# Optimization experiments

Measured on AMD Instinct MI355X. Metric: run time of the kernel, lower is better.

Reference implementation:

```python
import jax, jax.numpy as jnp
import numpy as np

DEPTH = 4
DIM = 1024
HEADS = 16
DIM_HEAD = 64
INNER = HEADS * DIM_HEAD  # 1024
MLP = 4096
CTX = 768
SCALE = DIM_HEAD ** -0.5
EPS = 1e-5


def setup_inputs() -> dict:
    key = jax.random.key(0)
    ks = jax.random.split(key, 12)
    def rn(k, shape, s=0.02):
        return jax.random.normal(k, shape, jnp.float32) * s
    return {
        "x": jax.random.normal(ks[0], (2, 2048, DIM), jnp.float32),
        "context": jax.random.normal(ks[1], (2, 1024, CTX), jnp.float32),
        "ln1_g": jnp.ones((DEPTH, DIM), jnp.float32),
        "ln1_b": jnp.zeros((DEPTH, DIM), jnp.float32),
        "w_qkv": rn(ks[2], (DEPTH, DIM, 3 * INNER)),
        "w_sa_o": rn(ks[3], (DEPTH, INNER, DIM)),
        "b_sa_o": jnp.zeros((DEPTH, DIM), jnp.float32),
        "ln2_g": jnp.ones((DEPTH, DIM), jnp.float32),
        "ln2_b": jnp.zeros((DEPTH, DIM), jnp.float32),
        "w_q": rn(ks[4], (DEPTH, DIM, INNER)),
        "w_kv": rn(ks[5], (DEPTH, CTX, 2 * INNER)),
        "w_ca_o": rn(ks[6], (DEPTH, INNER, DIM)),
        "b_ca_o": jnp.zeros((DEPTH, DIM), jnp.float32),
        "ln3_g": jnp.ones((DEPTH, DIM), jnp.float32),
        "ln3_b": jnp.zeros((DEPTH, DIM), jnp.float32),
        "w_ff1": rn(ks[7], (DEPTH, DIM, MLP)),
        "b_ff1": jnp.zeros((DEPTH, MLP), jnp.float32),
        "w_ff2": rn(ks[8], (DEPTH, MLP, DIM)),
        "b_ff2": jnp.zeros((DEPTH, DIM), jnp.float32),
    }


def _ln(x, g, b):
    mu = jnp.mean(x, axis=-1, keepdims=True)
    var = jnp.mean(jnp.square(x - mu), axis=-1, keepdims=True)
    return (x - mu) * jax.lax.rsqrt(var + EPS) * g + b


def _heads(t):
    # [b, n, h*d] -> [b, h, n, d]
    b, n, _ = t.shape
    return t.reshape(b, n, HEADS, DIM_HEAD).transpose(0, 2, 1, 3)


def _mha(q, k, v):
    # q,k,v: [b, h, n, d]; naive matmul-softmax-matmul, same math as the torch code
    attn = jax.nn.softmax(jnp.einsum('bhqd,bhkd->bhqk', q, k) * SCALE, axis=-1)
    out = jnp.einsum('bhqk,bhkd->bhqd', attn, v)
    b, h, n, d = out.shape
    return out.transpose(0, 2, 1, 3).reshape(b, n, h * d)


def reference(x, context, ln1_g, ln1_b, w_qkv, w_sa_o, b_sa_o,
              ln2_g, ln2_b, w_q, w_kv, w_ca_o, b_ca_o,
              ln3_g, ln3_b, w_ff1, b_ff1, w_ff2, b_ff2):
    for i in range(DEPTH):
        # self-attention
        h = _ln(x, ln1_g[i], ln1_b[i])
        qkv = h @ w_qkv[i]
        q, k, v = jnp.split(qkv, 3, axis=-1)
        sa = _mha(_heads(q), _heads(k), _heads(v)) @ w_sa_o[i] + b_sa_o[i]
        x = sa + x
        # cross-attention
        h = _ln(x, ln2_g[i], ln2_b[i])
        q = h @ w_q[i]
        kv = context @ w_kv[i]
        k, v = jnp.split(kv, 2, axis=-1)
        ca = _mha(_heads(q), _heads(k), _heads(v)) @ w_ca_o[i] + b_ca_o[i]
        x = ca + x
        # feed-forward (exact GELU, matching torch nn.GELU default)
        h = _ln(x, ln3_g[i], ln3_b[i])
        ff = jax.nn.gelu(h @ w_ff1[i] + b_ff1[i], approximate=False) @ w_ff2[i] + b_ff2[i]
        x = ff + x
    return x
```

## Files before the change

kernel.cpp:

```cpp
#include <hip/hip_runtime.h>
#include <hip/hip_bf16.h>
#include <math.h>

typedef __bf16 bf16_t;
typedef __bf16 bf16x8 __attribute__((ext_vector_type(8)));
typedef __bf16 bf16x4 __attribute__((ext_vector_type(4)));
typedef float f32x4 __attribute__((ext_vector_type(4)));
typedef float f32x16 __attribute__((ext_vector_type(16)));
typedef unsigned short u16;
typedef unsigned int u32;
typedef u16 u16x8 __attribute__((ext_vector_type(8)));
typedef u32 u32x4 __attribute__((ext_vector_type(4)));

#define NDEPTH 4
#define DIM 1024
#define NHEADS 16
#define MLP_DIM 4096
#define CTXD 768
#define NTOK 4096
#define NCTX 2048
#define ATT_SC2 0.18033688011112042f

__device__ inline void gload_lds16(const void* g, void* l) {
  __builtin_amdgcn_global_load_lds(
      (const __attribute__((address_space(1))) void*)g,
      (__attribute__((address_space(3))) void*)l, 16, 0, 0);
}

__device__ inline u32 packbf2(float a, float b) {
  union { bf16_t h[2]; u32 w; } u;
  u.h[0] = (bf16_t)a; u.h[1] = (bf16_t)b;
  return u.w;
}

template<int EPI>
__device__ inline void epi_store(void* outp, const float* bias, const float* res,
                                 int row, int col, int N, float v) {
  size_t idx = (size_t)row * N + col;
  if (EPI == 3) {
    ((float*)outp)[idx] = v + bias[col] + res[idx];
  } else if (EPI == 2) {
    float vb = v + bias[col];
    ((bf16_t*)outp)[idx] = (bf16_t)(0.5f * vb * (1.f + erff(vb * 0.70710678118f)));
  } else {
    ((bf16_t*)outp)[idx] = (bf16_t)v;
  }
}

template<int EPI>
__global__ __launch_bounds__(512) void gemm_bf16(
    const bf16_t* __restrict__ A, const bf16_t* __restrict__ Bt,
    const float* __restrict__ bias, const float* __restrict__ res,
    void* __restrict__ outp, int M, int N, int K)
{
  __shared__ alignas(16) bf16_t As[3][128 * 32];
  __shared__ alignas(16) bf16_t Bs[3][128 * 32];
  const int tid = threadIdx.x, lane = tid & 63, wave = tid >> 6;
  const int bx = blockIdx.x, by = blockIdx.y;
  const int wr = wave >> 2, wc = wave & 3;
  const int l15 = lane & 15, l4 = lane >> 4;

  const bf16_t* Ag = A + (size_t)by * 128 * K;
  const bf16_t* Bg = Bt + (size_t)bx * 128 * K;

  f32x4 acc[4][2] = {};

  const int srow = tid >> 2, soff = (tid & 3) * 8;
  auto stage = [&](int buf, int k0) {
    gload_lds16(Ag + (size_t)srow * K + k0 + soff, &As[buf][(size_t)tid * 8]);
    gload_lds16(Bg + (size_t)srow * K + k0 + soff, &Bs[buf][(size_t)tid * 8]);
  };

  const int nk = K >> 5;
  stage(0, 0);
  stage(1, 32);
  asm volatile("s_waitcnt vmcnt(2)" ::: "memory");
  __builtin_amdgcn_s_barrier();
  __builtin_amdgcn_sched_barrier(0);

  for (int t = 0; t < nk; ++t) {
    const int cur = t % 3;
    if (t + 2 < nk) stage((t + 2) % 3, (t + 2) << 5);

    bf16x8 af[4], bfr[2];
#pragma unroll
    for (int mi = 0; mi < 4; ++mi)
      af[mi] = *(const bf16x8*)&As[cur][(wr * 64 + mi * 16 + l15) * 32 + l4 * 8];
#pragma unroll
    for (int ni = 0; ni < 2; ++ni)
      bfr[ni] = *(const bf16x8*)&Bs[cur][(wc * 32 + ni * 16 + l15) * 32 + l4 * 8];
#pragma unroll
    for (int mi = 0; mi < 4; ++mi)
#pragma unroll
      for (int ni = 0; ni < 2; ++ni)
        acc[mi][ni] = __builtin_amdgcn_mfma_f32_16x16x32_bf16(af[mi], bfr[ni], acc[mi][ni], 0, 0, 0);

    if (t + 2 < nk) {
      asm volatile("s_waitcnt vmcnt(2)" ::: "memory");
    } else if (t + 1 < nk) {
      asm volatile("s_waitcnt vmcnt(0)" ::: "memory");
    } else {
      break;
    }
    __builtin_amdgcn_s_barrier();
    __builtin_amdgcn_sched_barrier(0);
  }

  const int r0 = by * 128 + wr * 64, c0 = bx * 128 + wc * 32;
#pragma unroll
  for (int ni = 0; ni < 2; ++ni)
#pragma unroll
    for (int mi = 0; mi < 4; ++mi)
#pragma unroll
      for (int r = 0; r < 4; ++r)
        epi_store<EPI>(outp, bias, res, r0 + mi * 16 + l4 * 4 + r,
                       c0 + ni * 16 + l15, N, acc[mi][ni][r]);
}

template<int EPI>
__global__ __launch_bounds__(256) void gemm64_bf16(
    const bf16_t* __restrict__ A, const bf16_t* __restrict__ Bt,
    const float* __restrict__ bias, const float* __restrict__ res,
    void* __restrict__ outp, int M, int N, int K)
{
  __shared__ alignas(16) bf16_t As[3][64 * 32];
  __shared__ alignas(16) bf16_t Bs[3][64 * 32];
  const int tid = threadIdx.x, lane = tid & 63, wave = tid >> 6;
  const int bx = blockIdx.x, by = blockIdx.y;
  const int wr = wave >> 1, wc = wave & 1;
  const int l15 = lane & 15, l4 = lane >> 4;

  const bf16_t* Ag = A + (size_t)by * 64 * K;
  const bf16_t* Bg = Bt + (size_t)bx * 64 * K;

  f32x4 acc[2][2] = {};

  const int srow = tid >> 2, soff = (tid & 3) * 8;
  auto stage = [&](int buf, int k0) {
    gload_lds16(Ag + (size_t)srow * K + k0 + soff, &As[buf][(size_t)tid * 8]);
    gload_lds16(Bg + (size_t)srow * K + k0 + soff, &Bs[buf][(size_t)tid * 8]);
  };

  const int nk = K >> 5;
  stage(0, 0);
  stage(1, 32);
  asm volatile("s_waitcnt vmcnt(2)" ::: "memory");
  __builtin_amdgcn_s_barrier();
  __builtin_amdgcn_sched_barrier(0);

  for (int t = 0; t < nk; ++t) {
    const int cur = t % 3;
    if (t + 2 < nk) stage((t + 2) % 3, (t + 2) << 5);

    bf16x8 af[2], bfr[2];
#pragma unroll
    for (int mi = 0; mi < 2; ++mi)
      af[mi] = *(const bf16x8*)&As[cur][(wr * 32 + mi * 16 + l15) * 32 + l4 * 8];
#pragma unroll
    for (int ni = 0; ni < 2; ++ni)
      bfr[ni] = *(const bf16x8*)&Bs[cur][(wc * 32 + ni * 16 + l15) * 32 + l4 * 8];
#pragma unroll
    for (int mi = 0; mi < 2; ++mi)
#pragma unroll
      for (int ni = 0; ni < 2; ++ni)
        acc[mi][ni] = __builtin_amdgcn_mfma_f32_16x16x32_bf16(af[mi], bfr[ni], acc[mi][ni], 0, 0, 0);

    if (t + 2 < nk) {
      asm volatile("s_waitcnt vmcnt(2)" ::: "memory");
    } else if (t + 1 < nk) {
      asm volatile("s_waitcnt vmcnt(0)" ::: "memory");
    } else {
      break;
    }
    __builtin_amdgcn_s_barrier();
    __builtin_amdgcn_sched_barrier(0);
  }

  const int r0 = by * 64 + wr * 32, c0 = bx * 64 + wc * 32;
#pragma unroll
  for (int ni = 0; ni < 2; ++ni)
#pragma unroll
    for (int mi = 0; mi < 2; ++mi)
#pragma unroll
      for (int r = 0; r < 4; ++r)
        epi_store<EPI>(outp, bias, res, r0 + mi * 16 + l4 * 4 + r,
                       c0 + ni * 16 + l15, N, acc[mi][ni][r]);
}

__global__ __launch_bounds__(256) void attn_fwd(
    const bf16_t* __restrict__ Q, int qs,
    const bf16_t* __restrict__ K, const bf16_t* __restrict__ V, int kvs,
    bf16_t* __restrict__ O, int os, int nq, int nk)
{
  __shared__ bf16_t Ks[2][64][72];
  __shared__ bf16_t Vt[2][64][72];

  const int tid = threadIdx.x, lane = tid & 63, wv = tid >> 6;
  const int l31 = lane & 31, hi = lane >> 5;
  const int h = blockIdx.y, bz = blockIdx.z;
  const size_t qrow0 = (size_t)bz * nq + (size_t)blockIdx.x * 128 + wv * 32;
  const bf16_t* Qb = Q + qrow0 * qs + h * 64;
  const bf16_t* Kb = K + (size_t)bz * nk * kvs + h * 64;
  const bf16_t* Vb = V + (size_t)bz * nk * kvs + h * 64;
  bf16_t* Ob = O + qrow0 * os + h * 64;

  bf16x8 qa[4];
#pragma unroll
  for (int c = 0; c < 4; ++c)
    qa[c] = *(const bf16x8*)(Qb + (size_t)l31 * qs + c * 16 + hi * 8);

  const int krow = tid >> 2, kcol = (tid & 3) * 16;
  const int vd = tid & 63, vkb = tid >> 6;

  u16x8 kreg[2], vreg[2];
  auto load_tile = [&](int kt) {
#pragma unroll
    for (int i = 0; i < 2; ++i)
      kreg[i] = *(const u16x8*)(Kb + (size_t)(kt * 64 + krow) * kvs + kcol + i * 8);
#pragma unroll
    for (int i = 0; i < 2; ++i) {
      u16x8 t;
#pragma unroll
      for (int j = 0; j < 8; ++j)
        t[j] = *(const u16*)(Vb + (size_t)(kt * 64 + vkb * 16 + i * 8 + j) * kvs + vd);
      vreg[i] = t;
    }
  };
  auto store_tile = [&](int buf) {
#pragma unroll
    for (int i = 0; i < 2; ++i)
      *(u16x8*)&Ks[buf][krow][kcol + i * 8] = kreg[i];
#pragma unroll
    for (int i = 0; i < 2; ++i)
      *(u16x8*)&Vt[buf][vd][vkb * 16 + i * 8] = vreg[i];
  };

  float m_run2 = -1e30f, l_run = 0.f;
  f32x16 acc[2] = {};

  const int ntiles = nk >> 6;
  load_tile(0);
  store_tile(0);
  __syncthreads();

  for (int kt = 0; kt < ntiles; ++kt) {
    const int cur = kt & 1;
    const bool pre = (kt + 1 < ntiles);
    if (pre) load_tile(kt + 1);

    f32x16 s[2] = {};
    __builtin_amdgcn_s_setprio(1);
#pragma unroll
    for (int kb = 0; kb < 2; ++kb)
#pragma unroll
      for (int c = 0; c < 4; ++c) {
        bf16x8 kf = *(const bf16x8*)&Ks[cur][kb * 32 + l31][c * 16 + hi * 8];
        s[kb] = __builtin_amdgcn_mfma_f32_32x32x16_bf16(kf, qa[c], s[kb], 0, 0, 0);
      }
    __builtin_amdgcn_s_setprio(0);

    float smax = s[0][0];
#pragma unroll
    for (int kb = 0; kb < 2; ++kb)
#pragma unroll
      for (int r = 0; r < 16; ++r) smax = fmaxf(smax, s[kb][r]);
    smax *= ATT_SC2;
    smax = fmaxf(smax, __shfl_xor(smax, 32));

    if (!__all(smax <= m_run2 + 11.0f)) {
      const float mn = fmaxf(m_run2, smax);
      const float esc = exp2f(m_run2 - mn);
      m_run2 = mn;
      l_run *= esc;
#pragma unroll
      for (int r = 0; r < 16; ++r) {
        int q = (r & 3) + 8 * (r >> 2) + 4 * hi;
        float eq = __shfl(esc, q);
        acc[0][r] *= eq;
        acc[1][r] *= eq;
      }
    }

    float psum = 0.f;
    u32x4 paw[2][2];
#pragma unroll
    for (int kb = 0; kb < 2; ++kb) {
      float pv[16];
#pragma unroll
      for (int r = 0; r < 16; ++r) {
        pv[r] = exp2f(s[kb][r] * ATT_SC2 - m_run2);
        psum += pv[r];
      }
#pragma unroll
      for (int h2 = 0; h2 < 2; ++h2) {
        u32 a0 = packbf2(pv[h2 * 8 + 0], pv[h2 * 8 + 1]);
        u32 a1 = packbf2(pv[h2 * 8 + 2], pv[h2 * 8 + 3]);
        u32 a2 = packbf2(pv[h2 * 8 + 4], pv[h2 * 8 + 5]);
        u32 a3 = packbf2(pv[h2 * 8 + 6], pv[h2 * 8 + 7]);
        asm volatile("v_permlane32_swap_b32 %0, %1" : "+v"(a0), "+v"(a2));
        asm volatile("v_permlane32_swap_b32 %0, %1" : "+v"(a1), "+v"(a3));
        paw[kb][h2][0] = a0; paw[kb][h2][1] = a1;
        paw[kb][h2][2] = a2; paw[kb][h2][3] = a3;
      }
    }
    psum += __shfl_xor(psum, 32);
    l_run += psum;

    __builtin_amdgcn_s_setprio(1);
#pragma unroll
    for (int kb = 0; kb < 2; ++kb)
#pragma unroll
      for (int h2 = 0; h2 < 2; ++h2) {
        union { u32x4 w; bf16x8 v; } pu;
        pu.w = paw[kb][h2];
#pragma unroll
        for (int dblk = 0; dblk < 2; ++dblk) {
          bf16x8 vb = *(const bf16x8*)&Vt[cur][dblk * 32 + l31][kb * 32 + h2 * 16 + hi * 8];
          acc[dblk] = __builtin_amdgcn_mfma_f32_32x32x16_bf16(pu.v, vb, acc[dblk], 0, 0, 0);
        }
      }
    __builtin_amdgcn_s_setprio(0);

    if (pre) store_tile(cur ^ 1);
    __syncthreads();
  }

#pragma unroll
  for (int r = 0; r < 16; ++r) {
    int q = (r & 3) + 8 * (r >> 2) + 4 * hi;
    float lq = __shfl(l_run, q);
    float inv = 1.f / lq;
#pragma unroll
    for (int dblk = 0; dblk < 2; ++dblk)
      Ob[(size_t)q * os + dblk * 32 + l31] = (bf16_t)(acc[dblk][r] * inv);
  }
}

__global__ __launch_bounds__(256) void layernorm_f32_bf16(
    const float* __restrict__ x, const float* __restrict__ g, const float* __restrict__ b,
    bf16_t* __restrict__ out)
{
  const int row = blockIdx.x, tid = threadIdx.x;
  const float4 v = ((const float4*)(x + (size_t)row * 1024))[tid];
  float s = v.x + v.y + v.z + v.w;
  float s2 = v.x * v.x + v.y * v.y + v.z * v.z + v.w * v.w;
#pragma unroll
  for (int off = 32; off > 0; off >>= 1) {
    s += __shfl_down(s, off);
    s2 += __shfl_down(s2, off);
  }
  __shared__ float ps[4], ps2[4];
  const int lane = tid & 63, wave = tid >> 6;
  if (lane == 0) { ps[wave] = s; ps2[wave] = s2; }
  __syncthreads();
  s = ps[0] + ps[1] + ps[2] + ps[3];
  s2 = ps2[0] + ps2[1] + ps2[2] + ps2[3];
  const float mu = s * (1.f / 1024.f);
  const float var = s2 * (1.f / 1024.f) - mu * mu;
  const float rstd = rsqrtf(var + 1e-5f);
  const float4 gv = ((const float4*)g)[tid];
  const float4 bv = ((const float4*)b)[tid];
  bf16x4 o;
  o[0] = (bf16_t)((v.x - mu) * rstd * gv.x + bv.x);
  o[1] = (bf16_t)((v.y - mu) * rstd * gv.y + bv.y);
  o[2] = (bf16_t)((v.z - mu) * rstd * gv.z + bv.z);
  o[3] = (bf16_t)((v.w - mu) * rstd * gv.w + bv.w);
  *(bf16x4*)(out + (size_t)row * 1024 + tid * 4) = o;
}

__global__ void transpose_to_bf16(const float* __restrict__ src, bf16_t* __restrict__ dst, int K, int N)
{
  __shared__ float tile[32][33];
  const size_t loff = (size_t)blockIdx.z * K * N;
  src += loff; dst += loff;
  const int k0 = blockIdx.y * 32, n0 = blockIdx.x * 32;
  const int tx = threadIdx.x, ty = threadIdx.y;
#pragma unroll
  for (int i = ty; i < 32; i += 8)
    tile[i][tx] = src[(size_t)(k0 + i) * N + n0 + tx];
  __syncthreads();
#pragma unroll
  for (int i = ty; i < 32; i += 8)
    dst[(size_t)(n0 + i) * K + k0 + tx] = (bf16_t)tile[tx][i];
}

__global__ void f32_to_bf16(const float* __restrict__ src, bf16_t* __restrict__ dst, int n4)
{
  int i = blockIdx.x * blockDim.x + threadIdx.x;
  if (i < n4) {
    float4 v = ((const float4*)src)[i];
    bf16x4 o;
    o[0] = (bf16_t)v.x; o[1] = (bf16_t)v.y; o[2] = (bf16_t)v.z; o[3] = (bf16_t)v.w;
    ((bf16x4*)dst)[i] = o;
  }
}

__global__ void copy_f32(const float* __restrict__ src, float* __restrict__ dst, int n4)
{
  int i = blockIdx.x * blockDim.x + threadIdx.x;
  if (i < n4) ((float4*)dst)[i] = ((const float4*)src)[i];
}

extern "C" void kernel_launch(void* const* d_in, const int* in_sizes, int n_in,
                              void* d_out, int out_size, void* d_ws, size_t ws_size,
                              hipStream_t stream)
{
  const float* x      = (const float*)d_in[0];
  const float* ctx    = (const float*)d_in[1];
  const float* ln1_g  = (const float*)d_in[2];
  const float* ln1_b  = (const float*)d_in[3];
  const float* w_qkv  = (const float*)d_in[4];
  const float* w_sa_o = (const float*)d_in[5];
  const float* b_sa_o = (const float*)d_in[6];
  const float* ln2_g  = (const float*)d_in[7];
  const float* ln2_b  = (const float*)d_in[8];
  const float* w_q    = (const float*)d_in[9];
  const float* w_kv   = (const float*)d_in[10];
  const float* w_ca_o = (const float*)d_in[11];
  const float* b_ca_o = (const float*)d_in[12];
  const float* ln3_g  = (const float*)d_in[13];
  const float* ln3_b  = (const float*)d_in[14];
  const float* w_ff1  = (const float*)d_in[15];
  const float* b_ff1  = (const float*)d_in[16];
  const float* w_ff2  = (const float*)d_in[17];
  const float* b_ff2  = (const float*)d_in[18];

  char* p = (char*)d_ws;
  auto alloc = [&](size_t bytes) { char* r = p; p += (bytes + 255) & ~(size_t)255; return r; };
  bf16_t* wqkv_t = (bf16_t*)alloc((size_t)NDEPTH * 3072 * 1024 * 2);
  bf16_t* wsao_t = (bf16_t*)alloc((size_t)NDEPTH * 1024 * 1024 * 2);
  bf16_t* wq_t   = (bf16_t*)alloc((size_t)NDEPTH * 1024 * 1024 * 2);
  bf16_t* wkv_t  = (bf16_t*)alloc((size_t)NDEPTH * 2048 * 768 * 2);
  bf16_t* wcao_t = (bf16_t*)alloc((size_t)NDEPTH * 1024 * 1024 * 2);
  bf16_t* wff1_t = (bf16_t*)alloc((size_t)NDEPTH * 4096 * 1024 * 2);
  bf16_t* wff2_t = (bf16_t*)alloc((size_t)NDEPTH * 1024 * 4096 * 2);
  bf16_t* ctxb   = (bf16_t*)alloc((size_t)NCTX * CTXD * 2);
  float*  xbuf   = (float*)alloc((size_t)NTOK * DIM * 4);
  bf16_t* lnbuf  = (bf16_t*)alloc((size_t)NTOK * DIM * 2);
  bf16_t* bigbuf = (bf16_t*)alloc((size_t)NTOK * 4096 * 2);
  bf16_t* qbuf   = (bf16_t*)alloc((size_t)NTOK * DIM * 2);
  bf16_t* kvbuf  = (bf16_t*)alloc((size_t)NCTX * 2048 * 2);
  if ((size_t)(p - (char*)d_ws) > ws_size) return;

  dim3 tb(32, 8);
  transpose_to_bf16<<<dim3(3072 / 32, 1024 / 32, NDEPTH), tb, 0, stream>>>(w_qkv, wqkv_t, 1024, 3072);
  transpose_to_bf16<<<dim3(1024 / 32, 1024 / 32, NDEPTH), tb, 0, stream>>>(w_sa_o, wsao_t, 1024, 1024);
  transpose_to_bf16<<<dim3(1024 / 32, 1024 / 32, NDEPTH), tb, 0, stream>>>(w_q, wq_t, 1024, 1024);
  transpose_to_bf16<<<dim3(2048 / 32, 768 / 32, NDEPTH), tb, 0, stream>>>(w_kv, wkv_t, 768, 2048);
  transpose_to_bf16<<<dim3(1024 / 32, 1024 / 32, NDEPTH), tb, 0, stream>>>(w_ca_o, wcao_t, 1024, 1024);
  transpose_to_bf16<<<dim3(4096 / 32, 1024 / 32, NDEPTH), tb, 0, stream>>>(w_ff1, wff1_t, 1024, 4096);
  transpose_to_bf16<<<dim3(1024 / 32, 4096 / 32, NDEPTH), tb, 0, stream>>>(w_ff2, wff2_t, 4096, 1024);
  f32_to_bf16<<<(NCTX * CTXD / 4 + 255) / 256, 256, 0, stream>>>(ctx, ctxb, NCTX * CTXD / 4);
  copy_f32<<<(NTOK * DIM / 4 + 255) / 256, 256, 0, stream>>>(x, xbuf, NTOK * DIM / 4);

  for (int i = 0; i < NDEPTH; ++i) {
    layernorm_f32_bf16<<<NTOK, 256, 0, stream>>>(xbuf, ln1_g + i * DIM, ln1_b + i * DIM, lnbuf);
    gemm_bf16<0><<<dim3(3072 / 128, NTOK / 128), 512, 0, stream>>>(
        lnbuf, wqkv_t + (size_t)i * 3072 * 1024, nullptr, nullptr, bigbuf, NTOK, 3072, 1024);
    attn_fwd<<<dim3(2048 / 128, NHEADS, 2), 256, 0, stream>>>(
        bigbuf, 3072, bigbuf + 1024, bigbuf + 2048, 3072, lnbuf, 1024, 2048, 2048);
    gemm64_bf16<3><<<dim3(1024 / 64, NTOK / 64), 256, 0, stream>>>(
        lnbuf, wsao_t + (size_t)i * 1024 * 1024, b_sa_o + i * DIM, xbuf, xbuf, NTOK, 1024, 1024);
    layernorm_f32_bf16<<<NTOK, 256, 0, stream>>>(xbuf, ln2_g + i * DIM, ln2_b + i * DIM, lnbuf);
    gemm64_bf16<0><<<dim3(1024 / 64, NTOK / 64), 256, 0, stream>>>(
        lnbuf, wq_t + (size_t)i * 1024 * 1024, nullptr, nullptr, qbuf, NTOK, 1024, 1024);
    gemm64_bf16<0><<<dim3(2048 / 64, NCTX / 64), 256, 0, stream>>>(
        ctxb, wkv_t + (size_t)i * 2048 * 768, nullptr, nullptr, kvbuf, NCTX, 2048, 768);
    attn_fwd<<<dim3(2048 / 128, NHEADS, 2), 256, 0, stream>>>(
        qbuf, 1024, kvbuf, kvbuf + 1024, 2048, lnbuf, 1024, 2048, 1024);
    gemm64_bf16<3><<<dim3(1024 / 64, NTOK / 64), 256, 0, stream>>>(
        lnbuf, wcao_t + (size_t)i * 1024 * 1024, b_ca_o + i * DIM, xbuf, xbuf, NTOK, 1024, 1024);
    layernorm_f32_bf16<<<NTOK, 256, 0, stream>>>(xbuf, ln3_g + i * DIM, ln3_b + i * DIM, lnbuf);
    gemm_bf16<2><<<dim3(4096 / 128, NTOK / 128), 512, 0, stream>>>(
        lnbuf, wff1_t + (size_t)i * 4096 * 1024, b_ff1 + i * MLP_DIM, nullptr, bigbuf, NTOK, 4096, 1024);
    gemm64_bf16<3><<<dim3(1024 / 64, NTOK / 64), 256, 0, stream>>>(
        bigbuf, wff2_t + (size_t)i * 1024 * 4096, b_ff2 + i * DIM, xbuf, xbuf, NTOK, 1024, 4096);
  }
  copy_f32<<<(NTOK * DIM / 4 + 255) / 256, 256, 0, stream>>>(xbuf, (float*)d_out, NTOK * DIM / 4);
}
```

Baseline: 1.830 ms.

## Split attention KV tiles across wave pairs and merge partial softmax states

```diff
diff --git a/kernel.cpp b/kernel.cpp
--- a/kernel.cpp
+++ b/kernel.cpp
@@ -197,8 +197,9 @@
 
   const int tid = threadIdx.x, lane = tid & 63, wv = tid >> 6;
   const int l31 = lane & 31, hi = lane >> 5;
+  const int pair = wv >> 1, sK = wv & 1;
   const int h = blockIdx.y, bz = blockIdx.z;
-  const size_t qrow0 = (size_t)bz * nq + (size_t)blockIdx.x * 128 + wv * 32;
+  const size_t qrow0 = (size_t)bz * nq + (size_t)blockIdx.x * 64 + pair * 32;
   const bf16_t* Qb = Q + qrow0 * qs + h * 64;
   const bf16_t* Kb = K + (size_t)bz * nk * kvs + h * 64;
   const bf16_t* Vb = V + (size_t)bz * nk * kvs + h * 64;
@@ -248,22 +249,18 @@
     const bool pre = (kt + 1 < ntiles);
     if (pre) load_tile(kt + 1);
 
-    f32x16 s[2] = {};
+    f32x16 s = {};
     __builtin_amdgcn_s_setprio(1);
 #pragma unroll
-    for (int kb = 0; kb < 2; ++kb)
-#pragma unroll
-      for (int c = 0; c < 4; ++c) {
-        bf16x8 kf = *(const bf16x8*)&Ks[cur][kb * 32 + l31][c * 16 + hi * 8];
-        s[kb] = __builtin_amdgcn_mfma_f32_32x32x16_bf16(kf, qa[c], s[kb], 0, 0, 0);
-      }
+    for (int c = 0; c < 4; ++c) {
+      bf16x8 kf = *(const bf16x8*)&Ks[cur][sK * 32 + l31][c * 16 + hi * 8];
+      s = __builtin_amdgcn_mfma_f32_32x32x16_bf16(kf, qa[c], s, 0, 0, 0);
+    }
     __builtin_amdgcn_s_setprio(0);
 
-    float smax = s[0][0];
-#pragma unroll
-    for (int kb = 0; kb < 2; ++kb)
-#pragma unroll
-      for (int r = 0; r < 16; ++r) smax = fmaxf(smax, s[kb][r]);
+    float smax = s[0];
+#pragma unroll
+    for (int r = 1; r < 16; ++r) smax = fmaxf(smax, s[r]);
     smax *= ATT_SC2;
     smax = fmaxf(smax, __shfl_xor(smax, 32));
 
@@ -282,57 +279,75 @@
     }
 
     float psum = 0.f;
-    u32x4 paw[2][2];
-#pragma unroll
-    for (int kb = 0; kb < 2; ++kb) {
-      float pv[16];
-#pragma unroll
-      for (int r = 0; r < 16; ++r) {
-        pv[r] = exp2f(s[kb][r] * ATT_SC2 - m_run2);
-        psum += pv[r];
-      }
-#pragma unroll
-      for (int h2 = 0; h2 < 2; ++h2) {
-        u32 a0 = packbf2(pv[h2 * 8 + 0], pv[h2 * 8 + 1]);
-        u32 a1 = packbf2(pv[h2 * 8 + 2], pv[h2 * 8 + 3]);
-        u32 a2 = packbf2(pv[h2 * 8 + 4], pv[h2 * 8 + 5]);
-        u32 a3 = packbf2(pv[h2 * 8 + 6], pv[h2 * 8 + 7]);
-        asm volatile("v_permlane32_swap_b32 %0, %1" : "+v"(a0), "+v"(a2));
-        asm volatile("v_permlane32_swap_b32 %0, %1" : "+v"(a1), "+v"(a3));
-        paw[kb][h2][0] = a0; paw[kb][h2][1] = a1;
-        paw[kb][h2][2] = a2; paw[kb][h2][3] = a3;
-      }
+    float pv[16];
+#pragma unroll
+    for (int r = 0; r < 16; ++r) {
+      pv[r] = exp2f(s[r] * ATT_SC2 - m_run2);
+      psum += pv[r];
     }
     psum += __shfl_xor(psum, 32);
     l_run += psum;
 
+    u32x4 paw[2];
+#pragma unroll
+    for (int h2 = 0; h2 < 2; ++h2) {
+      u32 a0 = packbf2(pv[h2 * 8 + 0], pv[h2 * 8 + 1]);
+      u32 a1 = packbf2(pv[h2 * 8 + 2], pv[h2 * 8 + 3]);
+      u32 a2 = packbf2(pv[h2 * 8 + 4], pv[h2 * 8 + 5]);
+      u32 a3 = packbf2(pv[h2 * 8 + 6], pv[h2 * 8 + 7]);
+      asm volatile("v_permlane32_swap_b32 %0, %1" : "+v"(a0), "+v"(a2));
+      asm volatile("v_permlane32_swap_b32 %0, %1" : "+v"(a1), "+v"(a3));
+      paw[h2][0] = a0; paw[h2][1] = a1; paw[h2][2] = a2; paw[h2][3] = a3;
+    }
+
     __builtin_amdgcn_s_setprio(1);
 #pragma unroll
-    for (int kb = 0; kb < 2; ++kb)
-#pragma unroll
-      for (int h2 = 0; h2 < 2; ++h2) {
-        union { u32x4 w; bf16x8 v; } pu;
-        pu.w = paw[kb][h2];
-#pragma unroll
-        for (int dblk = 0; dblk < 2; ++dblk) {
-          bf16x8 vb = *(const bf16x8*)&Vt[cur][dblk * 32 + l31][kb * 32 + h2 * 16 + hi * 8];
-          acc[dblk] = __builtin_amdgcn_mfma_f32_32x32x16_bf16(pu.v, vb, acc[dblk], 0, 0, 0);
-        }
+    for (int h2 = 0; h2 < 2; ++h2) {
+      union { u32x4 w; bf16x8 v; } pu;
+      pu.w = paw[h2];
+#pragma unroll
+      for (int dblk = 0; dblk < 2; ++dblk) {
+        bf16x8 vb = *(const bf16x8*)&Vt[cur][dblk * 32 + l31][sK * 32 + h2 * 16 + hi * 8];
+        acc[dblk] = __builtin_amdgcn_mfma_f32_32x32x16_bf16(pu.v, vb, acc[dblk], 0, 0, 0);
       }
+    }
     __builtin_amdgcn_s_setprio(0);
 
     if (pre) store_tile(cur ^ 1);
     __syncthreads();
   }
 
-#pragma unroll
-  for (int r = 0; r < 16; ++r) {
-    int q = (r & 3) + 8 * (r >> 2) + 4 * hi;
-    float lq = __shfl(l_run, q);
-    float inv = 1.f / lq;
+  float* mb = (float*)&Ks[0][0][0];
+  float* ml = (float*)&Vt[0][0][0];
+  if (sK == 1) {
 #pragma unroll
     for (int dblk = 0; dblk < 2; ++dblk)
-      Ob[(size_t)q * os + dblk * 32 + l31] = (bf16_t)(acc[dblk][r] * inv);
+#pragma unroll
+      for (int r = 0; r < 16; ++r)
+        mb[((pair * 2 + dblk) * 16 + r) * 64 + lane] = acc[dblk][r];
+    if (lane < 32) {
+      ml[(pair * 2 + 0) * 32 + lane] = m_run2;
+      ml[(pair * 2 + 1) * 32 + lane] = l_run;
+    }
+  }
+  __syncthreads();
+  if (sK == 0) {
+    float m1 = ml[(pair * 2 + 0) * 32 + l31];
+    float l1 = ml[(pair * 2 + 1) * 32 + l31];
+    float mm = fmaxf(m_run2, m1);
+    float f0 = exp2f(m_run2 - mm), f1 = exp2f(m1 - mm);
+    float inv = 1.f / (l_run * f0 + l1 * f1);
+#pragma unroll
+    for (int r = 0; r < 16; ++r) {
+      int q = (r & 3) + 8 * (r >> 2) + 4 * hi;
+      float f0r = __shfl(f0, q), f1r = __shfl(f1, q), invr = __shfl(inv, q);
+#pragma unroll
+      for (int dblk = 0; dblk < 2; ++dblk) {
+        float o = (acc[dblk][r] * f0r +
+                   mb[((pair * 2 + dblk) * 16 + r) * 64 + lane] * f1r) * invr;
+        Ob[(size_t)q * os + dblk * 32 + l31] = (bf16_t)o;
+      }
+    }
   }
 }
 
@@ -457,7 +472,7 @@
     layernorm_f32_bf16<<<NTOK, 256, 0, stream>>>(xbuf, ln1_g + i * DIM, ln1_b + i * DIM, lnbuf);
     gemm_bf16<0><<<dim3(3072 / 128, NTOK / 128), 512, 0, stream>>>(
         lnbuf, wqkv_t + (size_t)i * 3072 * 1024, nullptr, nullptr, bigbuf, NTOK, 3072, 1024);
-    attn_fwd<<<dim3(2048 / 128, NHEADS, 2), 256, 0, stream>>>(
+    attn_fwd<<<dim3(2048 / 64, NHEADS, 2), 256, 0, stream>>>(
         bigbuf, 3072, bigbuf + 1024, bigbuf + 2048, 3072, lnbuf, 1024, 2048, 2048);
     gemm64_bf16<3><<<dim3(1024 / 64, NTOK / 64), 256, 0, stream>>>(
         lnbuf, wsao_t + (size_t)i * 1024 * 1024, b_sa_o + i * DIM, xbuf, xbuf, NTOK, 1024, 1024);
@@ -466,7 +481,7 @@
         lnbuf, wq_t + (size_t)i * 1024 * 1024, nullptr, nullptr, qbuf, NTOK, 1024, 1024);
     gemm64_bf16<0><<<dim3(2048 / 64, NCTX / 64), 256, 0, stream>>>(
         ctxb, wkv_t + (size_t)i * 2048 * 768, nullptr, nullptr, kvbuf, NCTX, 2048, 768);
-    attn_fwd<<<dim3(2048 / 128, NHEADS, 2), 256, 0, stream>>>(
+    attn_fwd<<<dim3(2048 / 64, NHEADS, 2), 256, 0, stream>>>(
         qbuf, 1024, kvbuf, kvbuf + 1024, 2048, lnbuf, 1024, 2048, 1024);
     gemm64_bf16<3><<<dim3(1024 / 64, NTOK / 64), 256, 0, stream>>>(
         lnbuf, wcao_t + (size_t)i * 1024 * 1024, b_ca_o + i * DIM, xbuf, xbuf, NTOK, 1024, 1024);
```

Measured after the change: 1.973 ms. +7.8%, slower.
